# Performance work log

Hardware: AMD Instinct MI355X
Metric: run time of the kernel (lower is better)

## Reference

```python
import jax, jax.numpy as jnp
import numpy as np

B = 32        # graphs per batch
N_PER = 128   # nodes per graph (n_max)
E_PER = 4096  # edges per graph
T_PER = 4096  # tokens per graph
D = 64        # embed_dim
N, E, T = B * N_PER, B * E_PER, B * T_PER


def setup_inputs() -> dict:
    key = jax.random.key(0)
    k = jax.random.split(key, 8)
    x = jax.random.normal(k[0], (N, D), jnp.float32)
    # intra-graph COO indices (PyG convention): global node ids, src/dst in same graph
    g_e = jnp.repeat(jnp.arange(B, dtype=jnp.int32), E_PER)
    src = jax.random.randint(k[1], (E,), 0, N_PER, dtype=jnp.int32) + g_e * N_PER
    dst = jax.random.randint(k[2], (E,), 0, N_PER, dtype=jnp.int32) + g_e * N_PER
    edge_index = jnp.stack([src, dst])
    edge_attr = jax.random.normal(k[3], (E, D), jnp.float32)
    g_t = jnp.repeat(jnp.arange(B, dtype=jnp.int32), T_PER)
    tsrc = jax.random.randint(k[4], (T,), 0, N_PER, dtype=jnp.int32) + g_t * N_PER
    tdst = jax.random.randint(k[5], (T,), 0, N_PER, dtype=jnp.int32) + g_t * N_PER
    token_index = jnp.stack([tsrc, tdst])
    batch = jnp.repeat(jnp.arange(B, dtype=jnp.int32), N_PER)
    # node_proj: Linear(2*D, D)
    W = jax.random.normal(k[6], (D, 2 * D), jnp.float32) / np.sqrt(2 * D)
    b = jax.random.normal(k[7], (D,), jnp.float32) * 0.01
    return {"x": x, "edge_index": edge_index, "edge_attr": edge_attr,
            "batch": batch, "token_index": token_index, "W": W, "b": b}


def _to_dense_adj(idx, batch, attr, ptr):
    # idx: [2, M] global node ids; attr: [M, F] -> dense [B, n_max, n_max, F]
    g = batch[idx[0]]
    row = idx[0] - ptr[g]
    col = idx[1] - ptr[g]
    out = jnp.zeros((B, N_PER, N_PER, attr.shape[-1]), attr.dtype)
    return out.at[g, row, col].add(attr)


def reference(x, edge_index, edge_attr, batch, token_index, W, b):
    # per-graph node offsets (ptr), as in PyG to_dense_adj
    counts = jax.ops.segment_sum(jnp.ones_like(batch), batch, num_segments=B)
    ptr = jnp.concatenate([jnp.zeros((1,), counts.dtype), jnp.cumsum(counts)[:-1]])
    edge_features = _to_dense_adj(edge_index, batch, edge_attr, ptr)  # [B,n,n,D]
    # gather endpoint features: x[token_index.T] -> [T, 2, D] -> [T, 2D]
    h = x[token_index.T].reshape(token_index.shape[1], 2 * D)
    h = h @ W.T + b  # node_proj (linear=True)
    xd = _to_dense_adj(token_index, batch, h, ptr)  # [B,n,n,D]
    return xd + edge_features
```

## Files before the change

kernel.cpp:

```cpp
#include <hip/hip_runtime.h>
#include <hip/hip_bf16.h>

#define N_NODES 4096
#define N_PER   128
#define D_DIM   64
#define CELLS   (N_NODES * N_PER)
#define CAP     12

__global__ void init_proj(int4* __restrict__ cp4,
                          const float* __restrict__ x,
                          const float* __restrict__ W,
                          const float* __restrict__ b,
                          float* __restrict__ p1,
                          float* __restrict__ p2) {
    if (blockIdx.x < 512) {
        int i = blockIdx.x * 256 + threadIdx.x;
        cp4[i] = make_int4(0, 0, 0, 0);
    } else {
        int n = (blockIdx.x - 512) * 4 + (threadIdx.x >> 6);
        int d = threadIdx.x & 63;
        const float* xr = x + (size_t)n * D_DIM;
        const float* w  = W + (size_t)d * (2 * D_DIM);
        float a1 = b[d];
        float a2 = 0.0f;
#pragma unroll
        for (int k = 0; k < D_DIM; ++k) {
            float xv = xr[k];
            a1 += xv * w[k];
            a2 += xv * w[D_DIM + k];
        }
        p1[(size_t)n * D_DIM + d] = a1;
        p2[(size_t)n * D_DIM + d] = a2;
    }
}

__global__ void link(const int* __restrict__ esrc,
                     const int* __restrict__ edst,
                     const int* __restrict__ tsrc,
                     const int* __restrict__ tdst,
                     int* __restrict__ cnt_pack,
                     int* __restrict__ cslots,
                     int E, int total) {
    int i = blockIdx.x * blockDim.x + threadIdx.x;
    if (i >= total) return;
    if (i < E) {
        int s = esrc[i];
        int cell = (s << 7) | (edst[i] & 127);
        int old = atomicAdd(&cnt_pack[cell], 0x10000);
        int slot = old >> 16;
        if (slot < CAP) cslots[(size_t)cell * CAP + slot] = i;
    } else {
        int j = i - E;
        int cell = (tsrc[j] << 7) | (tdst[j] & 127);
        atomicAdd(&cnt_pack[cell], 1);
    }
}

__global__ void __launch_bounds__(256, 8)
row_write(const int* __restrict__ cnt_pack,
          const int* __restrict__ cslots,
          const float4* __restrict__ attr4,
          const float4* __restrict__ p14,
          const float4* __restrict__ p24,
          float4* __restrict__ out4) {
    const int k      = blockIdx.x;
    const int gbase  = k & ~127;
    const int wave   = threadIdx.x >> 6;
    const int grp    = (threadIdx.x >> 4) & 3;
    const int lane16 = threadIdx.x & 15;
    const int cbase  = wave * 32;

    float4 p1v = p14[(size_t)k * 16 + lane16];

    int pk[8];
#pragma unroll
    for (int it = 0; it < 8; ++it)
        pk[it] = cnt_pack[(k << 7) + cbase + it * 4 + grp];

#pragma unroll
    for (int it = 0; it < 8; ++it) {
        int c    = cbase + it * 4 + grp;
        int cell = (k << 7) | c;
        float f  = (float)(pk[it] & 0xFFFF);
        float4 p2v = p24[(size_t)(gbase | c) * 16 + lane16];
        float4 v;
        v.x = f * (p1v.x + p2v.x);
        v.y = f * (p1v.y + p2v.y);
        v.z = f * (p1v.z + p2v.z);
        v.w = f * (p1v.w + p2v.w);
        int n = pk[it] >> 16;
        if (n > CAP) n = CAP;
        const int* sl = cslots + (size_t)cell * CAP;
        for (int i = 0; i < n; ++i) {
            int e = sl[i];
            float4 a = attr4[(size_t)e * 16 + lane16];
            v.x += a.x; v.y += a.y; v.z += a.z; v.w += a.w;
        }
        out4[(size_t)cell * 16 + lane16] = v;
    }
}

extern "C" void kernel_launch(void* const* d_in, const int* in_sizes, int n_in,
                              void* d_out, int out_size, void* d_ws, size_t ws_size,
                              hipStream_t stream) {
    const float* x           = (const float*)d_in[0];
    const int*   edge_index  = (const int*)d_in[1];
    const float* edge_attr   = (const float*)d_in[2];
    const int*   token_index = (const int*)d_in[4];
    const float* W           = (const float*)d_in[5];
    const float* b           = (const float*)d_in[6];

    const int E = in_sizes[1] / 2;
    const int T = in_sizes[4] / 2;

    float* p1       = (float*)d_ws;
    float* p2       = p1 + (size_t)N_NODES * D_DIM;
    int*   cnt_pack = (int*)(p2 + (size_t)N_NODES * D_DIM);
    int*   cslots   = cnt_pack + CELLS;

    init_proj<<<1536, 256, 0, stream>>>((int4*)cnt_pack, x, W, b, p1, p2);

    int total = E + T;
    link<<<(total + 255) / 256, 256, 0, stream>>>(
        edge_index, edge_index + E, token_index, token_index + T,
        cnt_pack, cslots, E, total);

    row_write<<<N_NODES, 256, 0, stream>>>(
        cnt_pack, cslots, (const float4*)edge_attr,
        (const float4*)p1, (const float4*)p2, (float4*)d_out);
}
```

Baseline: 69.92 us.

## Permute edge attributes into per-row buckets and accumulate in shared memory

Instead of storing per-cell edge index slots and gathering edge_attr rows randomly in the output kernel, the link pass now buckets edges by source row (capacity 128 per row) and copies their attribute vectors contiguously into a row-sorted buffer. The row kernel then scatters these into a 128x64 LDS tile with shared-memory atomics before combining them with the token projection term. This targets the scattered global gathers and the per-cell loop divergence, at the cost of an extra write and read of the full edge-attribute array, LDS atomics, and lower occupancy (launch bounds 4). Rows with more than 128 edges would silently drop contributions, and the hard-coded grid sizes assume the fixed E and T.

After: 123.4 us. 1.76x slower.

```diff
diff --git a/kernel.cpp b/kernel.cpp
--- a/kernel.cpp
+++ b/kernel.cpp
@@ -5,19 +5,20 @@
 #define N_PER   128
 #define D_DIM   64
 #define CELLS   (N_NODES * N_PER)
-#define CAP     12
+#define RCAP    128
 
-__global__ void init_proj(int4* __restrict__ cp4,
+__global__ void init_proj(int4* __restrict__ cnt4, int4* __restrict__ ecnt4,
                           const float* __restrict__ x,
                           const float* __restrict__ W,
                           const float* __restrict__ b,
                           float* __restrict__ p1,
                           float* __restrict__ p2) {
-    if (blockIdx.x < 512) {
+    if (blockIdx.x < 516) {
         int i = blockIdx.x * 256 + threadIdx.x;
-        cp4[i] = make_int4(0, 0, 0, 0);
+        if (i < 131072)              cnt4[i] = make_int4(0, 0, 0, 0);
+        else if (i < 131072 + 1024)  ecnt4[i - 131072] = make_int4(0, 0, 0, 0);
     } else {
-        int n = (blockIdx.x - 512) * 4 + (threadIdx.x >> 6);
+        int n = (blockIdx.x - 516) * 4 + (threadIdx.x >> 6);
         int d = threadIdx.x & 63;
         const float* xr = x + (size_t)n * D_DIM;
         const float* w  = W + (size_t)d * (2 * D_DIM);
@@ -34,69 +35,89 @@
     }
 }
 
-__global__ void link(const int* __restrict__ esrc,
-                     const int* __restrict__ edst,
-                     const int* __restrict__ tsrc,
-                     const int* __restrict__ tdst,
-                     int* __restrict__ cnt_pack,
-                     int* __restrict__ cslots,
-                     int E, int total) {
-    int i = blockIdx.x * blockDim.x + threadIdx.x;
-    if (i >= total) return;
-    if (i < E) {
-        int s = esrc[i];
-        int cell = (s << 7) | (edst[i] & 127);
-        int old = atomicAdd(&cnt_pack[cell], 0x10000);
-        int slot = old >> 16;
-        if (slot < CAP) cslots[(size_t)cell * CAP + slot] = i;
+__global__ void link_permute(const int* __restrict__ esrc,
+                             const int* __restrict__ edst,
+                             const int* __restrict__ tsrc,
+                             const int* __restrict__ tdst,
+                             const float4* __restrict__ attr4,
+                             int* __restrict__ ecnt_row,
+                             int* __restrict__ ecol_s,
+                             float4* __restrict__ eattr_s,
+                             int* __restrict__ cnt) {
+    if (blockIdx.x < 8192) {
+        int grp    = threadIdx.x >> 4;
+        int lane16 = threadIdx.x & 15;
+        int e = blockIdx.x * 16 + grp;
+        int s = esrc[e];
+        int c = edst[e] & 127;
+        int slot = 0;
+        if (lane16 == 0) slot = atomicAdd(&ecnt_row[s], 1);
+        slot = __shfl(slot, threadIdx.x & 48, 64);
+        if (slot < RCAP) {
+            size_t dst = (size_t)s * RCAP + slot;
+            eattr_s[dst * 16 + lane16] = attr4[(size_t)e * 16 + lane16];
+            if (lane16 == 0) ecol_s[dst] = c;
+        }
     } else {
-        int j = i - E;
+        int j = (blockIdx.x - 8192) * 256 + threadIdx.x;
         int cell = (tsrc[j] << 7) | (tdst[j] & 127);
-        atomicAdd(&cnt_pack[cell], 1);
+        atomicAdd(&cnt[cell], 1);
     }
 }
 
-__global__ void __launch_bounds__(256, 8)
-row_write(const int* __restrict__ cnt_pack,
-          const int* __restrict__ cslots,
-          const float4* __restrict__ attr4,
+__global__ void __launch_bounds__(256, 4)
+row_write(const int* __restrict__ cnt,
+          const int* __restrict__ ecnt_row,
+          const int* __restrict__ ecol_s,
+          const float4* __restrict__ eattr_s,
           const float4* __restrict__ p14,
           const float4* __restrict__ p24,
           float4* __restrict__ out4) {
+    __shared__ float lds[N_PER * D_DIM];
     const int k      = blockIdx.x;
     const int gbase  = k & ~127;
     const int wave   = threadIdx.x >> 6;
-    const int grp    = (threadIdx.x >> 4) & 3;
+    const int grp16  = threadIdx.x >> 4;
+    const int grp    = grp16 & 3;
     const int lane16 = threadIdx.x & 15;
-    const int cbase  = wave * 32;
 
-    float4 p1v = p14[(size_t)k * 16 + lane16];
+    float4* l4 = (float4*)lds;
+#pragma unroll
+    for (int it = 0; it < 8; ++it)
+        l4[it * 256 + threadIdx.x] = make_float4(0.f, 0.f, 0.f, 0.f);
+    __syncthreads();
 
+    int n = ecnt_row[k];
+    if (n > RCAP) n = RCAP;
+    for (int i = grp16; i < n; i += 16) {
+        int c = ecol_s[k * RCAP + i];
+        float4 a = eattr_s[((size_t)k * RCAP + i) * 16 + lane16];
+        atomicAdd(&lds[c * 64 + lane16 * 4 + 0], a.x);
+        atomicAdd(&lds[c * 64 + lane16 * 4 + 1], a.y);
+        atomicAdd(&lds[c * 64 + lane16 * 4 + 2], a.z);
+        atomicAdd(&lds[c * 64 + lane16 * 4 + 3], a.w);
+    }
+    __syncthreads();
+
+    const int cbase = wave * 32;
     int pk[8];
 #pragma unroll
     for (int it = 0; it < 8; ++it)
-        pk[it] = cnt_pack[(k << 7) + cbase + it * 4 + grp];
+        pk[it] = cnt[(k << 7) + cbase + it * 4 + grp];
+    float4 p1v = p14[(size_t)k * 16 + lane16];
 
 #pragma unroll
     for (int it = 0; it < 8; ++it) {
-        int c    = cbase + it * 4 + grp;
-        int cell = (k << 7) | c;
-        float f  = (float)(pk[it] & 0xFFFF);
+        int c = cbase + it * 4 + grp;
+        float f = (float)pk[it];
         float4 p2v = p24[(size_t)(gbase | c) * 16 + lane16];
+        float4 l = l4[c * 16 + lane16];
         float4 v;
-        v.x = f * (p1v.x + p2v.x);
-        v.y = f * (p1v.y + p2v.y);
-        v.z = f * (p1v.z + p2v.z);
-        v.w = f * (p1v.w + p2v.w);
-        int n = pk[it] >> 16;
-        if (n > CAP) n = CAP;
-        const int* sl = cslots + (size_t)cell * CAP;
-        for (int i = 0; i < n; ++i) {
-            int e = sl[i];
-            float4 a = attr4[(size_t)e * 16 + lane16];
-            v.x += a.x; v.y += a.y; v.z += a.z; v.w += a.w;
-        }
-        out4[(size_t)cell * 16 + lane16] = v;
+        v.x = f * (p1v.x + p2v.x) + l.x;
+        v.y = f * (p1v.y + p2v.y) + l.y;
+        v.z = f * (p1v.z + p2v.z) + l.z;
+        v.w = f * (p1v.w + p2v.w) + l.w;
+        out4[(size_t)((k << 7) | c) * 16 + lane16] = v;
     }
 }
 
@@ -112,20 +133,23 @@
 
     const int E = in_sizes[1] / 2;
     const int T = in_sizes[4] / 2;
+    (void)E; (void)T;
 
     float* p1       = (float*)d_ws;
     float* p2       = p1 + (size_t)N_NODES * D_DIM;
-    int*   cnt_pack = (int*)(p2 + (size_t)N_NODES * D_DIM);
-    int*   cslots   = cnt_pack + CELLS;
+    int*   cnt      = (int*)(p2 + (size_t)N_NODES * D_DIM);
+    int*   ecnt_row = cnt + CELLS;
+    int*   ecol_s   = ecnt_row + N_NODES;
+    float* eattr_s  = (float*)(ecol_s + N_NODES * RCAP);
+    
+    init_proj<<<1540, 256, 0, stream>>>((int4*)cnt, (int4*)ecnt_row,
+                                        x, W, b, p1, p2);
 
-    init_proj<<<1536, 256, 0, stream>>>((int4*)cnt_pack, x, W, b, p1, p2);
-
-    int total = E + T;
-    link<<<(total + 255) / 256, 256, 0, stream>>>(
+    link_permute<<<8704, 256, 0, stream>>>(
         edge_index, edge_index + E, token_index, token_index + T,
-        cnt_pack, cslots, E, total);
+        (const float4*)edge_attr, ecnt_row, ecol_s, (float4*)eattr_s, cnt);
 
     row_write<<<N_NODES, 256, 0, stream>>>(
-        cnt_pack, cslots, (const float4*)edge_attr,
+        cnt, ecnt_row, ecol_s, (const float4*)eattr_s,
         (const float4*)p1, (const float4*)p2, (float4*)d_out);
 }
```
